# Kernel optimization log

Measured on AMD Instinct MI355X. Metric: run time of the kernel, lower is better.

Reference implementation:

```python
import jax, jax.numpy as jnp
import numpy as np

BSZ, D = 64, 65536
N_NODES, N_FEATS, EMBED_DIM = 1024, 256, 256


def setup_inputs() -> dict:
    key = jax.random.key(0)
    k1, k2, k3, k4, k5, k6 = jax.random.split(key, 6)
    flat_inputs = jax.random.normal(k1, (BSZ, D), dtype=jnp.float32)
    node_ids = jax.random.randint(k2, (BSZ, D), 0, N_NODES, dtype=jnp.int64 if jax.config.jax_enable_x64 else jnp.int32)
    feat_ids = jax.random.randint(k3, (BSZ, D), 0, N_FEATS, dtype=jnp.int64 if jax.config.jax_enable_x64 else jnp.int32)
    # Linear(n_feats -> embed_dim): W is (embed_dim, n_feats) like torch, plus bias.
    lim = 1.0 / np.sqrt(N_FEATS)
    W = jax.random.uniform(k4, (EMBED_DIM, N_FEATS), minval=-lim, maxval=lim, dtype=jnp.float32)
    b = jax.random.uniform(k5, (EMBED_DIM,), minval=-lim, maxval=lim, dtype=jnp.float32)
    global_emb = jax.random.normal(k6, (N_NODES, EMBED_DIM), dtype=jnp.float32)
    return {"flat_inputs": flat_inputs, "node_ids": node_ids, "feat_ids": feat_ids,
            "W": W, "b": b, "global_emb": global_emb}


def _expand(vals, node_ids, feat_ids, n_nodes, n_feats):
    # scatter-fill a dense (bsz, n_nodes, n_feats) tensor (zeros elsewhere)
    bsz, d = vals.shape
    batch_ids = jnp.broadcast_to(jnp.arange(bsz)[:, None], (bsz, d))
    out = jnp.zeros((bsz, n_nodes, n_feats), dtype=vals.dtype)
    return out.at[batch_ids.ravel(), node_ids.ravel(), feat_ids.ravel()].set(vals.ravel())


def reference(flat_inputs, node_ids, feat_ids, W, b, global_emb):
    obs_mat = _expand(flat_inputs, node_ids, feat_ids, N_NODES, N_FEATS)
    mask_mat = _expand(jnp.ones_like(flat_inputs), node_ids, feat_ids, N_NODES, N_FEATS)
    obs_counts = mask_mat.sum(-1, keepdims=True)            # (bsz, n_nodes, 1)
    obs_masked = jnp.nan_to_num((obs_mat * mask_mat) / obs_counts)
    missing_node_mask = obs_counts == 0
    # nodewise Linear + global embedding broadcast over batch
    embedded = jnp.einsum('bnf,ef->bne', obs_masked, W) + b + global_emb[None, :, :]
    return embedded, missing_node_mask
```

## Files before the change

kernel.cpp:

```cpp
#include <hip/hip_runtime.h>
#include <hip/hip_bf16.h>

#define BSZ    64
#define DLEN   65536
#define NNODES 1024
#define NFEATS 256
#define EDIM   256
#define NROWS  (BSZ * NNODES)

#define NRANGE  16
#define NBUCKET (BSZ * NRANGE)
#define LCAP    400
#define GCAP    4600
#define WPAD    268

typedef __bf16 bf16x8 __attribute__((ext_vector_type(8)));
typedef float  f32x4  __attribute__((ext_vector_type(4)));

__device__ __forceinline__ unsigned short f2bf(float x) {
  union { float f; unsigned u; } c; c.f = x;
  unsigned r = c.u + 0x7FFFu + ((c.u >> 16) & 1u);
  return (unsigned short)(r >> 16);
}

__global__ __launch_bounds__(256) void wconv_kernel(
    const float* __restrict__ W, unsigned short* __restrict__ Wb) {
  int i = (blockIdx.x * 256 + threadIdx.x) * 4;
  float4 w = *(const float4*)(W + i);
  ushort4 o;
  o.x = f2bf(w.x); o.y = f2bf(w.y); o.z = f2bf(w.z); o.w = f2bf(w.w);
  *(ushort4*)(Wb + i) = o;
}

__global__ __launch_bounds__(256) void bucket_kernel(
    const float* __restrict__ x, const int* __restrict__ nid,
    const int* __restrict__ fid, unsigned* __restrict__ gcnt,
    uint2* __restrict__ gbuf) {
  __shared__ uint2 lbuf[NRANGE][LCAP];
  __shared__ unsigned lcnt[NRANGE];
  __shared__ unsigned lbase[NRANGE];

  const int t = threadIdx.x;
  if (t < NRANGE) lcnt[t] = 0;
  __syncthreads();

  const int b = blockIdx.x >> 4;
  const int base = blockIdx.x * 4096;

  for (int k = 0; k < 16; ++k) {
    int i = base + k * 256 + t;
    int node = nid[i];
    int feat = fid[i];
    float v  = x[i];
    int d = i & 0xFFFF;
    unsigned pack = (((unsigned)(d + 1)) << 15) | ((unsigned)f2bf(v) >> 1);
    int r = node >> 6;
    unsigned row = (unsigned)(node & 63);
    uint2 rec;
    rec.x = pack;
    rec.y = (row << 16) | (row * WPAD + (unsigned)feat);
    unsigned li = atomicAdd(&lcnt[r], 1u);
    if (li < LCAP) {
      lbuf[r][li] = rec;
    } else {
      unsigned gi = atomicAdd(&gcnt[b * NRANGE + r], 1u);
      if (gi < GCAP) gbuf[(size_t)(b * NRANGE + r) * GCAP + gi] = rec;
    }
  }
  __syncthreads();

  if (t < NRANGE) {
    unsigned n = lcnt[t]; if (n > LCAP) n = LCAP;
    lcnt[t] = n;
    lbase[t] = atomicAdd(&gcnt[b * NRANGE + t], n);
  }
  __syncthreads();

  for (int r = 0; r < NRANGE; ++r) {
    unsigned n  = lcnt[r];
    unsigned bs = lbase[r];
    uint2* dst = gbuf + (size_t)(b * NRANGE + r) * GCAP;
    for (unsigned j = t; j < n; j += 256) {
      unsigned gi = bs + j;
      if (gi < GCAP) dst[gi] = lbuf[r][j];
    }
  }
}

__global__ __launch_bounds__(256) void fused_kernel(
    const unsigned* __restrict__ gcnt, const uint2* __restrict__ gbuf,
    const unsigned short* __restrict__ Wb, const float* __restrict__ bias,
    const float* __restrict__ gemb,
    float* __restrict__ out_emb, float* __restrict__ out_mask) {
  __shared__ __align__(16) unsigned win[64 * WPAD];
  __shared__ int counts[64];
  __shared__ float scl[64];

  const int t = threadIdx.x;
  const int g = blockIdx.x;
  const int row0 = g * 64;
  const int nb = (g & 15) * 64;

  uint4* wz = (uint4*)win;
#pragma unroll
  for (int j = t; j < (64 * WPAD) / 4; j += 256) wz[j] = make_uint4(0u, 0u, 0u, 0u);
  if (t < 64) counts[t] = 0;
  __syncthreads();

  int cn = (int)gcnt[g]; if (cn > GCAP) cn = GCAP;
  const uint2* bk = gbuf + (size_t)g * GCAP;
  for (int j = t; j < cn; j += 256) {
    uint2 rec = bk[j];
    unsigned idx = rec.y & 0xFFFFu;
    unsigned row = rec.y >> 16;
    unsigned old = atomicMax(&win[idx], rec.x);
    if (old == 0u) atomicAdd(&counts[row], 1);
  }
  __syncthreads();

  if (t < 64) {
    int c = counts[t];
    scl[t] = c ? 1.0f / (float)c : 0.0f;
    out_mask[row0 + t] = c ? 0.0f : 1.0f;
  }

  const int wv   = t >> 6;
  const int lane = t & 63;
  const int cl   = lane & 15;
  const int q    = lane >> 4;
  const int col0 = wv * 64;

  f32x4 acc[4][4];
#pragma unroll
  for (int mt = 0; mt < 4; ++mt)
#pragma unroll
    for (int nt = 0; nt < 4; ++nt) acc[mt][nt] = (f32x4)(0.0f);

#pragma unroll
  for (int ks = 0; ks < 8; ++ks) {
    bf16x8 bfr[4];
#pragma unroll
    for (int nt = 0; nt < 4; ++nt) {
      const uint4* wp = (const uint4*)(Wb + (size_t)(col0 + nt * 16 + cl) * NFEATS + ks * 32 + q * 8);
      bfr[nt] = __builtin_bit_cast(bf16x8, *wp);
    }
#pragma unroll
    for (int mt = 0; mt < 4; ++mt) {
      const uint4* ap = (const uint4*)&win[(mt * 16 + cl) * WPAD + ks * 32 + q * 8];
      uint4 lo = ap[0], hi = ap[1];
      uint4 pk;
      pk.x = ((lo.x & 0x7FFFu) << 1) | ((lo.y & 0x7FFFu) << 17);
      pk.y = ((lo.z & 0x7FFFu) << 1) | ((lo.w & 0x7FFFu) << 17);
      pk.z = ((hi.x & 0x7FFFu) << 1) | ((hi.y & 0x7FFFu) << 17);
      pk.w = ((hi.z & 0x7FFFu) << 1) | ((hi.w & 0x7FFFu) << 17);
      bf16x8 afr = __builtin_bit_cast(bf16x8, pk);
#pragma unroll
      for (int nt = 0; nt < 4; ++nt)
        acc[mt][nt] = __builtin_amdgcn_mfma_f32_16x16x32_bf16(afr, bfr[nt], acc[mt][nt], 0, 0, 0);
    }
  }
  __syncthreads();

#pragma unroll
  for (int nt = 0; nt < 4; ++nt) {
    int col = col0 + nt * 16 + cl;
    float bv = bias[col];
#pragma unroll
    for (int mt = 0; mt < 4; ++mt) {
#pragma unroll
      for (int r2 = 0; r2 < 4; ++r2) {
        int row = mt * 16 + q * 4 + r2;
        float o = acc[mt][nt][r2] * scl[row] + bv + gemb[(size_t)(nb + row) * EDIM + col];
        out_emb[(size_t)(row0 + row) * EDIM + col] = o;
      }
    }
  }
}

extern "C" void kernel_launch(void* const* d_in, const int* in_sizes, int n_in,
                              void* d_out, int out_size, void* d_ws, size_t ws_size,
                              hipStream_t stream) {
  const float* x    = (const float*)d_in[0];
  const int*   nid  = (const int*)d_in[1];
  const int*   fid  = (const int*)d_in[2];
  const float* W    = (const float*)d_in[3];
  const float* bias = (const float*)d_in[4];
  const float* gemb = (const float*)d_in[5];

  float* out_emb  = (float*)d_out;
  float* out_mask = out_emb + (size_t)NROWS * EDIM;

  unsigned* gcnt = (unsigned*)d_ws;
  uint2* gbuf = (uint2*)((char*)d_ws + 8192);
  unsigned short* Wb = (unsigned short*)((char*)d_ws + 8192 + (size_t)NBUCKET * GCAP * sizeof(uint2));

  hipMemsetAsync(gcnt, 0, NBUCKET * sizeof(unsigned), stream);
  wconv_kernel<<<64, 256, 0, stream>>>(W, Wb);
  bucket_kernel<<<(BSZ * DLEN) / 4096, 256, 0, stream>>>(x, nid, fid, gcnt, gbuf);
  fused_kernel<<<NBUCKET, 256, 0, stream>>>(gcnt, gbuf, Wb, bias, gemb, out_emb, out_mask);
}
```

Baseline: 173.8 us.

## Widen blocks to 512 threads, vectorize bucket loads, fold memset into conversion kernel

Several changes land together. The separate memset of bucket counters is folded into the weight conversion kernel, which saves one launch. The bucket kernel now runs 512 threads and reads float4/int4 vectors. The fused kernel runs 512 threads, with each wave owning 32 output columns instead of 64, and reads records in pairs. LCAP is lowered to fit occupancy hints, which may push more records through global atomics, and the smaller per-wave tiles cut the reuse of each A fragment.

```diff
diff --git a/kernel.cpp b/kernel.cpp
--- a/kernel.cpp
+++ b/kernel.cpp
@@ -10,7 +10,7 @@
 
 #define NRANGE  16
 #define NBUCKET (BSZ * NRANGE)
-#define LCAP    400
+#define LCAP    320
 #define GCAP    4600
 #define WPAD    268
 
@@ -24,15 +24,17 @@
 }
 
 __global__ __launch_bounds__(256) void wconv_kernel(
-    const float* __restrict__ W, unsigned short* __restrict__ Wb) {
+    const float* __restrict__ W, unsigned short* __restrict__ Wb,
+    unsigned* __restrict__ gcnt) {
   int i = (blockIdx.x * 256 + threadIdx.x) * 4;
   float4 w = *(const float4*)(W + i);
   ushort4 o;
   o.x = f2bf(w.x); o.y = f2bf(w.y); o.z = f2bf(w.z); o.w = f2bf(w.w);
   *(ushort4*)(Wb + i) = o;
-}
-
-__global__ __launch_bounds__(256) void bucket_kernel(
+  if (blockIdx.x == 0) ((uint4*)gcnt)[threadIdx.x] = make_uint4(0u, 0u, 0u, 0u);
+}
+
+__global__ __launch_bounds__(512, 6) void bucket_kernel(
     const float* __restrict__ x, const int* __restrict__ nid,
     const int* __restrict__ fid, unsigned* __restrict__ gcnt,
     uint2* __restrict__ gbuf) {
@@ -47,24 +49,31 @@
   const int b = blockIdx.x >> 4;
   const int base = blockIdx.x * 4096;
 
-  for (int k = 0; k < 16; ++k) {
-    int i = base + k * 256 + t;
-    int node = nid[i];
-    int feat = fid[i];
-    float v  = x[i];
-    int d = i & 0xFFFF;
-    unsigned pack = (((unsigned)(d + 1)) << 15) | ((unsigned)f2bf(v) >> 1);
-    int r = node >> 6;
-    unsigned row = (unsigned)(node & 63);
-    uint2 rec;
-    rec.x = pack;
-    rec.y = (row << 16) | (row * WPAD + (unsigned)feat);
-    unsigned li = atomicAdd(&lcnt[r], 1u);
-    if (li < LCAP) {
-      lbuf[r][li] = rec;
-    } else {
-      unsigned gi = atomicAdd(&gcnt[b * NRANGE + r], 1u);
-      if (gi < GCAP) gbuf[(size_t)(b * NRANGE + r) * GCAP + gi] = rec;
+#pragma unroll
+  for (int k = 0; k < 2; ++k) {
+    int i = base + (k * 512 + t) * 4;
+    float4 xv = *(const float4*)(x + i);
+    int4   nv = *(const int4*)(nid + i);
+    int4   fv = *(const int4*)(fid + i);
+    int   nd[4] = {nv.x, nv.y, nv.z, nv.w};
+    int   ft[4] = {fv.x, fv.y, fv.z, fv.w};
+    float vl[4] = {xv.x, xv.y, xv.z, xv.w};
+#pragma unroll
+    for (int j = 0; j < 4; ++j) {
+      int d = (i + j) & 0xFFFF;
+      unsigned pack = (((unsigned)(d + 1)) << 15) | ((unsigned)f2bf(vl[j]) >> 1);
+      int r = nd[j] >> 6;
+      unsigned row = (unsigned)(nd[j] & 63);
+      uint2 rec;
+      rec.x = pack;
+      rec.y = (row << 16) | (row * WPAD + (unsigned)ft[j]);
+      unsigned li = atomicAdd(&lcnt[r], 1u);
+      if (li < LCAP) {
+        lbuf[r][li] = rec;
+      } else {
+        unsigned gi = atomicAdd(&gcnt[b * NRANGE + r], 1u);
+        if (gi < GCAP) gbuf[(size_t)(b * NRANGE + r) * GCAP + gi] = rec;
+      }
     }
   }
   __syncthreads();
@@ -80,14 +89,14 @@
     unsigned n  = lcnt[r];
     unsigned bs = lbase[r];
     uint2* dst = gbuf + (size_t)(b * NRANGE + r) * GCAP;
-    for (unsigned j = t; j < n; j += 256) {
+    for (unsigned j = t; j < n; j += 512) {
       unsigned gi = bs + j;
       if (gi < GCAP) dst[gi] = lbuf[r][j];
     }
   }
 }
 
-__global__ __launch_bounds__(256) void fused_kernel(
+__global__ __launch_bounds__(512, 4) void fused_kernel(
     const unsigned* __restrict__ gcnt, const uint2* __restrict__ gbuf,
     const unsigned short* __restrict__ Wb, const float* __restrict__ bias,
     const float* __restrict__ gemb,
@@ -102,19 +111,25 @@
   const int nb = (g & 15) * 64;
 
   uint4* wz = (uint4*)win;
-#pragma unroll
-  for (int j = t; j < (64 * WPAD) / 4; j += 256) wz[j] = make_uint4(0u, 0u, 0u, 0u);
+  for (int j = t; j < (64 * WPAD) / 4; j += 512) wz[j] = make_uint4(0u, 0u, 0u, 0u);
   if (t < 64) counts[t] = 0;
   __syncthreads();
 
   int cn = (int)gcnt[g]; if (cn > GCAP) cn = GCAP;
   const uint2* bk = gbuf + (size_t)g * GCAP;
-  for (int j = t; j < cn; j += 256) {
-    uint2 rec = bk[j];
-    unsigned idx = rec.y & 0xFFFFu;
-    unsigned row = rec.y >> 16;
-    unsigned old = atomicMax(&win[idx], rec.x);
-    if (old == 0u) atomicAdd(&counts[row], 1);
+  const uint4* bk4 = (const uint4*)bk;
+  int np = cn >> 1;
+  for (int j = t; j < np; j += 512) {
+    uint4 rr = bk4[j];
+    unsigned old0 = atomicMax(&win[rr.y & 0xFFFFu], rr.x);
+    if (old0 == 0u) atomicAdd(&counts[rr.y >> 16], 1);
+    unsigned old1 = atomicMax(&win[rr.w & 0xFFFFu], rr.z);
+    if (old1 == 0u) atomicAdd(&counts[rr.w >> 16], 1);
+  }
+  if ((cn & 1) && t == 0) {
+    uint2 rec = bk[cn - 1];
+    unsigned old = atomicMax(&win[rec.y & 0xFFFFu], rec.x);
+    if (old == 0u) atomicAdd(&counts[rec.y >> 16], 1);
   }
   __syncthreads();
 
@@ -128,19 +143,19 @@
   const int lane = t & 63;
   const int cl   = lane & 15;
   const int q    = lane >> 4;
-  const int col0 = wv * 64;
-
-  f32x4 acc[4][4];
+  const int col0 = wv * 32;
+
+  f32x4 acc[4][2];
 #pragma unroll
   for (int mt = 0; mt < 4; ++mt)
 #pragma unroll
-    for (int nt = 0; nt < 4; ++nt) acc[mt][nt] = (f32x4)(0.0f);
+    for (int nt = 0; nt < 2; ++nt) acc[mt][nt] = (f32x4)(0.0f);
 
 #pragma unroll
   for (int ks = 0; ks < 8; ++ks) {
-    bf16x8 bfr[4];
-#pragma unroll
-    for (int nt = 0; nt < 4; ++nt) {
+    bf16x8 bfr[2];
+#pragma unroll
+    for (int nt = 0; nt < 2; ++nt) {
       const uint4* wp = (const uint4*)(Wb + (size_t)(col0 + nt * 16 + cl) * NFEATS + ks * 32 + q * 8);
       bfr[nt] = __builtin_bit_cast(bf16x8, *wp);
     }
@@ -155,14 +170,14 @@
       pk.w = ((hi.z & 0x7FFFu) << 1) | ((hi.w & 0x7FFFu) << 17);
       bf16x8 afr = __builtin_bit_cast(bf16x8, pk);
 #pragma unroll
-      for (int nt = 0; nt < 4; ++nt)
+      for (int nt = 0; nt < 2; ++nt)
         acc[mt][nt] = __builtin_amdgcn_mfma_f32_16x16x32_bf16(afr, bfr[nt], acc[mt][nt], 0, 0, 0);
     }
   }
   __syncthreads();
 
 #pragma unroll
-  for (int nt = 0; nt < 4; ++nt) {
+  for (int nt = 0; nt < 2; ++nt) {
     int col = col0 + nt * 16 + cl;
     float bv = bias[col];
 #pragma unroll
@@ -194,8 +209,7 @@
   uint2* gbuf = (uint2*)((char*)d_ws + 8192);
   unsigned short* Wb = (unsigned short*)((char*)d_ws + 8192 + (size_t)NBUCKET * GCAP * sizeof(uint2));
 
-  hipMemsetAsync(gcnt, 0, NBUCKET * sizeof(unsigned), stream);
-  wconv_kernel<<<64, 256, 0, stream>>>(W, Wb);
-  bucket_kernel<<<(BSZ * DLEN) / 4096, 256, 0, stream>>>(x, nid, fid, gcnt, gbuf);
-  fused_kernel<<<NBUCKET, 256, 0, stream>>>(gcnt, gbuf, Wb, bias, gemb, out_emb, out_mask);
-}
+  wconv_kernel<<<64, 256, 0, stream>>>(W, Wb, gcnt);
+  bucket_kernel<<<(BSZ * DLEN) / 4096, 512, 0, stream>>>(x, nid, fid, gcnt, gbuf);
+  fused_kernel<<<NBUCKET, 512, 0, stream>>>(gcnt, gbuf, Wb, bias, gemb, out_emb, out_mask);
+}
```

Measured after the change: 148.3 us. 1.17x faster.
